# Optimization experiments

Measured on AMD Instinct MI355X. Metric: run time of the kernel, lower is better.

## Reference

```python
import jax, jax.numpy as jnp
import numpy as np

QLEN, KLEN, BSZ, NHEAD, DHEAD = 1024, 1024, 2, 16, 64
RLEN = QLEN + KLEN
SCALE = 1.0 / np.sqrt(DHEAD).astype(np.float32)  # 1/sqrt(d_head)


def setup_inputs() -> dict:
    key = jax.random.key(0)
    ks = jax.random.split(key, 10)
    return {
        "q_head": jax.random.normal(ks[0], (QLEN, BSZ, NHEAD, DHEAD), jnp.float32),
        "k_head_h": jax.random.normal(ks[1], (KLEN, BSZ, NHEAD, DHEAD), jnp.float32),
        "v_head_h": jax.random.normal(ks[2], (KLEN, BSZ, NHEAD, DHEAD), jnp.float32),
        "k_head_r": jax.random.normal(ks[3], (RLEN, BSZ, NHEAD, DHEAD), jnp.float32),
        "seg_embed": jax.random.normal(ks[4], (2, NHEAD, DHEAD), jnp.float32),
        "seg_mat": jax.random.uniform(ks[5], (QLEN, KLEN, BSZ, 2), jnp.float32),
        "r_w_bias": jax.random.normal(ks[6], (NHEAD, DHEAD), jnp.float32),
        "r_r_bias": jax.random.normal(ks[7], (NHEAD, DHEAD), jnp.float32),
        "r_s_bias": jax.random.normal(ks[8], (NHEAD, DHEAD), jnp.float32),
        "attn_mask": jnp.zeros((QLEN, KLEN, 1, 1), jnp.float32),
    }


def _rel_shift(x, klen):
    # x: [qlen, rlen, bsz, n_head] -> [qlen, klen, bsz, n_head]
    x = jnp.transpose(x, (1, 0, 2, 3))[1:]          # drop first position row
    x = jnp.transpose(x, (1, 0, 2, 3))[:, :klen]    # keep first klen columns
    return x


def reference(q_head, k_head_h, v_head_h, k_head_r, seg_embed, seg_mat,
              r_w_bias, r_r_bias, r_s_bias, attn_mask):
    # content-based score
    ac = jnp.einsum('ibnd,jbnd->ijbn', q_head + r_w_bias, k_head_h)
    # position-based score with relative shift
    bd = jnp.einsum('ibnd,jbnd->ijbn', q_head + r_r_bias, k_head_r)
    bd = _rel_shift(bd, klen=ac.shape[1])
    # segment-based score
    ef = jnp.einsum('ibnd,snd->ibns', q_head + r_s_bias, seg_embed)
    ef = jnp.einsum('ijbs,ibns->ijbn', seg_mat, ef)
    attn_score = (ac + bd + ef) * SCALE
    attn_score = attn_score - 1e30 * attn_mask
    attn_prob = jax.nn.softmax(attn_score, axis=1)  # over key dim j
    attn_vec = jnp.einsum('ijbn,jbnd->ibnd', attn_prob, v_head_h)
    return attn_vec
```

## Files before the change

kernel.cpp:

```cpp
#include <hip/hip_runtime.h>

#define QLEN 1024
#define KLEN 1024
#define BSZ 2
#define NHEAD 16
#define DHEAD 64
#define RS 2048
#define BLK_I 64
#define BLK_J 32
#define NT32 (KLEN / BLK_J)
#define NBN (BSZ * NHEAD)

#define SC2f  0.18033688011112440f
#define MBIGf 1.4426950408889634e30f

#define SEGP_BYTES  16777216u
#define KT_BYTES    ((size_t)NBN * NT32 * 4096)

typedef __attribute__((ext_vector_type(8))) short s16x8;
typedef __attribute__((ext_vector_type(8))) unsigned short u16x8;
typedef __attribute__((ext_vector_type(4))) unsigned short u16x4;
typedef __attribute__((ext_vector_type(4))) float f32x4;
typedef __attribute__((ext_vector_type(2))) float f32x2;

__device__ __forceinline__ unsigned short f2bf(float f) {
    union { float f; unsigned int u; } x; x.f = f;
    unsigned int r = x.u + 0x7fffu + ((x.u >> 16) & 1u);
    return (unsigned short)(r >> 16);
}
__device__ __forceinline__ float bf2f(unsigned short h) {
    union { unsigned int u; float f; } x; x.u = ((unsigned int)h) << 16;
    return x.f;
}

typedef const __attribute__((address_space(1))) unsigned int* gas_t;
typedef __attribute__((address_space(3))) unsigned int* las_t;
__device__ __forceinline__ void gl_lds16(const void* g, void* l) {
    __builtin_amdgcn_global_load_lds((gas_t)g, (las_t)l, 16, 0, 0);
}

__global__ __launch_bounds__(256)
void pack_all_kernel(const float* __restrict__ segmat,
                     const float* __restrict__ mask,
                     const float* __restrict__ kh,
                     const float* __restrict__ kr,
                     const float* __restrict__ v,
                     unsigned short* __restrict__ segT,
                     unsigned short* __restrict__ Kp,
                     unsigned short* __restrict__ Krp,
                     unsigned short* __restrict__ Vtp)
{
    __shared__ float smS[16][32][4];
    __shared__ float smM[16][33];
    __shared__ float VT[32][65];
    const int bid = blockIdx.x;
    const int tid = threadIdx.x;

    if (bid < 2048) {
        const int istrip = bid >> 5;
        const int jt     = bid & 31;
        const int ib     = istrip * 16;
        const int jb     = jt * 32;
        {
            const int il = tid >> 4;
            const int j2 = (tid & 15) * 2;
            const float* sp = segmat + ((size_t)(ib + il) * KLEN + jb + j2) * 4;
            *(f32x4*)&smS[il][j2][0]     = *(const f32x4*)sp;
            *(f32x4*)&smS[il][j2 + 1][0] = *(const f32x4*)(sp + 4);
            const float* mp = mask + (size_t)(ib + il) * KLEN + jb + j2;
            smM[il][j2]     = mp[0] * MBIGf;
            smM[il][j2 + 1] = mp[1] * MBIGf;
        }
        __syncthreads();
        const int k  = tid >> 6;
        const int l  = tid & 63;
        const int q4 = l >> 4;
        const int il = l & 15;
        const int jl = (k >> 1) * 16 + q4 * 4 + (k & 1) * 2;
#pragma unroll
        for (int b = 0; b < 2; ++b) {
            u16x8 o;
#pragma unroll
            for (int e = 0; e < 2; ++e) {
                o[e * 4 + 0] = f2bf(smS[il][jl + e][b * 2]);
                o[e * 4 + 1] = f2bf(smS[il][jl + e][b * 2 + 1]);
                o[e * 4 + 2] = f2bf(smM[il][jl + e]);
                o[e * 4 + 3] = 0;
            }
            unsigned short* op = segT + ((size_t)(b * 64 + istrip) << 16)
                                 + (jt << 11) + tid * 8;
            *(u16x8*)op = o;
        }
    } else {
        const int blk = bid - 2048;
        const int bn  = blk >> 5;
        const int jt  = blk & (NT32 - 1);
        const int b   = bn & 1;
        const int n   = bn >> 1;
        const int boff = b * NHEAD * DHEAD + n * DHEAD;
        const int j0  = jt * BLK_J;

        {
            const int j  = tid >> 3;
            const int dq = (tid & 7) * 8;
            const float* vp = v + (size_t)(j0 + j) * RS + boff + dq;
#pragma unroll
            for (int e = 0; e < 8; ++e) VT[j][dq + e] = vp[e];
        }
        __syncthreads();

        const size_t tb = (size_t)blk * 2048;
        {
            const int row = tid >> 3;
            const int ch  = (tid & 7) ^ (row & 7);
            u16x8 ok, orr;
            const float* hp = kh + (size_t)(j0 + row) * RS + boff + ch * 8;
            const float* rp = kr + (size_t)(j0 + row + 1) * RS + boff + ch * 8;
#pragma unroll
            for (int e = 0; e < 8; ++e) { ok[e] = f2bf(hp[e]); orr[e] = f2bf(rp[e]); }
            *(u16x8*)&Kp [tb + (size_t)tid * 8] = ok;
            *(u16x8*)&Krp[tb + (size_t)tid * 8] = orr;
        }
        {
            const int d  = tid >> 2;
            const int g  = tid & 3;
            const int ch = g ^ (d & 3);
            u16x8 ov;
#pragma unroll
            for (int e = 0; e < 8; ++e) ov[e] = f2bf(VT[ch * 8 + e][d]);
            *(u16x8*)&Vtp[tb + (size_t)tid * 8] = ov;
        }
    }
}

__global__ __launch_bounds__(256, 2)
void relattn_kernel(const float* __restrict__ q,
                    const float* __restrict__ segemb,
                    const float* __restrict__ rwb,
                    const float* __restrict__ rrb,
                    const float* __restrict__ rsb,
                    const unsigned short* __restrict__ segT,
                    const unsigned short* __restrict__ Kp,
                    const unsigned short* __restrict__ Krp,
                    const unsigned short* __restrict__ Vtp,
                    float* __restrict__ out)
{
    __shared__ unsigned short KhL[2][32][64];
    __shared__ unsigned short KrL[2][32][64];
    __shared__ unsigned short VtL[2][64][32];
    __shared__ unsigned short PlP[4][16][40];

    const int F = blockIdx.x;
    const int x = F & 7;
    const int k = F >> 3;
    const int g = (k >> 4) * 8 + x;
    const int i0 = (g >> 1) * BLK_I;
    const int b  = g & 1;
    const int n  = k & 15;
    const int bn = n * 2 + b;
    const int boff = b * NHEAD * DHEAD + n * DHEAD;

    const int tid  = threadIdx.x;
    const int wave = tid >> 6;
    const int lane = tid & 63;
    const int q4   = lane >> 4;
    const int c    = lane & 15;
    const int iRow = i0 + wave * 16 + c;

    s16x8 qwf[2], qrf[2];
    float e0, e1;
    {
        const float* qp = q + (size_t)iRow * RS + boff;
        float es0 = 0.f, es1 = 0.f;
#pragma unroll
        for (int kk = 0; kk < 2; ++kk) {
            const int off = kk * 32 + q4 * 8;
            const f32x4 q0 = *(const f32x4*)(qp + off);
            const f32x4 q1 = *(const f32x4*)(qp + off + 4);
            const f32x4 w0 = *(const f32x4*)(rwb + n * DHEAD + off);
            const f32x4 w1 = *(const f32x4*)(rwb + n * DHEAD + off + 4);
            const f32x4 r0 = *(const f32x4*)(rrb + n * DHEAD + off);
            const f32x4 r1 = *(const f32x4*)(rrb + n * DHEAD + off + 4);
            const f32x4 sa = *(const f32x4*)(segemb + n * DHEAD + off);
            const f32x4 sb = *(const f32x4*)(segemb + n * DHEAD + off + 4);
            const f32x4 ta = *(const f32x4*)(segemb + (NHEAD + n) * DHEAD + off);
            const f32x4 tb = *(const f32x4*)(segemb + (NHEAD + n) * DHEAD + off + 4);
            const f32x4 ra = *(const f32x4*)(rsb + n * DHEAD + off);
            const f32x4 rb = *(const f32x4*)(rsb + n * DHEAD + off + 4);
            s16x8 tw, tr;
#pragma unroll
            for (int e = 0; e < 4; ++e) {
                tw[e]     = (short)f2bf(q0[e] + w0[e]);
                tw[4 + e] = (short)f2bf(q1[e] + w1[e]);
                tr[e]     = (short)f2bf(q0[e] + r0[e]);
                tr[4 + e] = (short)f2bf(q1[e] + r1[e]);
                es0 += (q0[e] + ra[e]) * sa[e] + (q1[e] + rb[e]) * sb[e];
                es1 += (q0[e] + ra[e]) * ta[e] + (q1[e] + rb[e]) * tb[e];
            }
            qwf[kk] = tw; qrf[kk] = tr;
        }
        es0 += __shfl_xor(es0, 16, 64); es0 += __shfl_xor(es0, 32, 64);
        es1 += __shfl_xor(es1, 16, 64); es1 += __shfl_xor(es1, 32, 64);
        e0 = es0 * SC2f; e1 = es1 * SC2f;
    }

    const int tbase = bn * NT32;
    auto stage = [&](int jt, int buf) {
        const size_t toff = ((size_t)(tbase + jt)) << 12;
        const int go = tid * 16;
        const int lo = wave * 1024;
        gl_lds16((const char*)Kp  + toff + go, (char*)&KhL[buf][0][0] + lo);
        gl_lds16((const char*)Krp + toff + go, (char*)&KrL[buf][0][0] + lo);
        gl_lds16((const char*)Vtp + toff + go, (char*)&VtL[buf][0][0] + lo);
    };

    stage(0, 0);
    __syncthreads();

    float m = -INFINITY, lsum = 0.f;
    f32x4 acc[4];
#pragma unroll
    for (int dt = 0; dt < 4; ++dt) acc[dt] = (f32x4)0.f;

    const unsigned short* segW = segT + ((size_t)(b * 64 + (i0 >> 4) + wave) << 16);

    int cur = 0;
    for (int jt = 0; jt < NT32; ++jt) {
        if (jt + 1 < NT32) stage(jt + 1, cur ^ 1);

        const unsigned short* st = segW + (jt << 11);
        u16x8 pg[2][2];
        pg[0][0] = *(const u16x8*)(st + lane * 8);
        pg[0][1] = *(const u16x8*)(st + 512 + lane * 8);
        pg[1][0] = *(const u16x8*)(st + 1024 + lane * 8);
        pg[1][1] = *(const u16x8*)(st + 1536 + lane * 8);

        f32x4 sjT[2];
        sjT[0] = (f32x4)0.f; sjT[1] = (f32x4)0.f;
        __builtin_amdgcn_s_setprio(1);
#pragma unroll
        for (int kk = 0; kk < 2; ++kk)
#pragma unroll
            for (int js = 0; js < 2; ++js) {
                const int row = js * 16 + c;
                const int pcK = ((kk * 4 + q4) ^ (c & 7)) * 8;
                const s16x8 khf = *(const s16x8*)&KhL[cur][row][pcK];
                const s16x8 krf = *(const s16x8*)&KrL[cur][row][pcK];
                sjT[js] = __builtin_amdgcn_mfma_f32_16x16x32_bf16(khf, qwf[kk], sjT[js], 0, 0, 0);
                sjT[js] = __builtin_amdgcn_mfma_f32_16x16x32_bf16(krf, qrf[kk], sjT[js], 0, 0, 0);
            }
        __builtin_amdgcn_s_setprio(0);

        float sc8[8];
#pragma unroll
        for (int js = 0; js < 2; ++js)
#pragma unroll
            for (int r = 0; r < 4; ++r) {
                const u16x8 g2 = pg[js][r >> 1];
                const int bb = (r & 1) * 4;
                sc8[js * 4 + r] = sjT[js][r] * SC2f
                                  + bf2f(g2[bb]) * e0 + bf2f(g2[bb + 1]) * e1
                                  - bf2f(g2[bb + 2]);
            }
        float mt = fmaxf(
            fmaxf(fmaxf(sc8[0], sc8[1]), fmaxf(sc8[2], sc8[3])),
            fmaxf(fmaxf(sc8[4], sc8[5]), fmaxf(sc8[6], sc8[7])));
        mt = fmaxf(mt, __shfl_xor(mt, 16, 64));
        mt = fmaxf(mt, __shfl_xor(mt, 32, 64));
        const float mn  = fmaxf(m, mt);
        const float scl = __builtin_amdgcn_exp2f(m - mn);
        m = mn;
#pragma unroll
        for (int dt = 0; dt < 4; ++dt) acc[dt] *= scl;
        float p[8], ps = 0.f;
#pragma unroll
        for (int e = 0; e < 8; ++e) {
            p[e] = __builtin_amdgcn_exp2f(sc8[e] - m);
            ps += p[e];
        }
        lsum = lsum * scl + ps;

#pragma unroll
        for (int js = 0; js < 2; ++js) {
            unsigned int wlo, whi;
            asm("v_cvt_pk_bf16_f32 %0, %1, %2" : "=v"(wlo) : "v"(p[js * 4 + 0]), "v"(p[js * 4 + 1]));
            asm("v_cvt_pk_bf16_f32 %0, %1, %2" : "=v"(whi) : "v"(p[js * 4 + 2]), "v"(p[js * 4 + 3]));
            uint2 wv; wv.x = wlo; wv.y = whi;
            *(uint2*)((char*)&PlP[wave][c][0] + js * 32 + q4 * 8) = wv;
        }
        const s16x8 pf = *(const s16x8*)&PlP[wave][c][q4 * 8];

        __builtin_amdgcn_s_setprio(1);
#pragma unroll
        for (int dt = 0; dt < 4; ++dt) {
            const s16x8 vf = *(const s16x8*)&VtL[cur][dt * 16 + c][(q4 ^ (c & 3)) * 8];
            acc[dt] = __builtin_amdgcn_mfma_f32_16x16x32_bf16(vf, pf, acc[dt], 0, 0, 0);
        }
        __builtin_amdgcn_s_setprio(0);

        __syncthreads();
        cur ^= 1;
    }

    lsum += __shfl_xor(lsum, 16, 64);
    lsum += __shfl_xor(lsum, 32, 64);

    {
        const float inv = 1.f / lsum;
        float* op = out + (size_t)iRow * RS + boff;
#pragma unroll
        for (int dt = 0; dt < 4; ++dt) {
            const f32x4 o = acc[dt] * inv;
            *(f32x4*)&op[dt * 16 + q4 * 4] = o;
        }
    }
}

extern "C" void kernel_launch(void* const* d_in, const int* in_sizes, int n_in,
                              void* d_out, int out_size, void* d_ws, size_t ws_size,
                              hipStream_t stream) {
    const float* q   = (const float*)d_in[0];
    const float* kh  = (const float*)d_in[1];
    const float* v   = (const float*)d_in[2];
    const float* kr  = (const float*)d_in[3];
    const float* se  = (const float*)d_in[4];
    const float* sm  = (const float*)d_in[5];
    const float* rwb = (const float*)d_in[6];
    const float* rrb = (const float*)d_in[7];
    const float* rsb = (const float*)d_in[8];
    const float* msk = (const float*)d_in[9];
    float* out = (float*)d_out;

    char* wsb = (char*)d_ws;
    unsigned short* segT = (unsigned short*)wsb;
    unsigned short* Kp   = (unsigned short*)(wsb + SEGP_BYTES);
    unsigned short* Krp  = (unsigned short*)(wsb + SEGP_BYTES + KT_BYTES);
    unsigned short* Vtp  = (unsigned short*)(wsb + SEGP_BYTES + 2 * KT_BYTES);

    pack_all_kernel<<<2048 + NBN * NT32, 256, 0, stream>>>(sm, msk, kh, kr, v,
                                                           segT, Kp, Krp, Vtp);
    relattn_kernel<<<512, 256, 0, stream>>>(q, se, rwb, rrb, rsb, segT, Kp, Krp, Vtp, out);
}
```

Before: 56.10 us.

## Split key range across two blocks with merge kernel and lazy softmax rescale

Adds a split-K (flash-decoding style) path. Each query tile's key range is divided between two blocks, which write partial outputs plus max/sum values to workspace, and a new merge kernel combines them. The grid doubles to 1024 blocks and occupancy is raised to 4 blocks per CU, to fill the GPU better with the original 512 blocks. The online softmax now skips the rescale unless the running max grows by more than a threshold. The costs are an extra kernel launch and a partial-result round-trip through global memory.

```diff
diff --git a/kernel.cpp b/kernel.cpp
--- a/kernel.cpp
+++ b/kernel.cpp
@@ -13,9 +13,12 @@
 
 #define SC2f  0.18033688011112440f
 #define MBIGf 1.4426950408889634e30f
+#define THRf  8.0f
 
 #define SEGP_BYTES  16777216u
 #define KT_BYTES    ((size_t)NBN * NT32 * 4096)
+#define OPART_BYTES 16777216u
+#define ML_BYTES    524288u
 
 typedef __attribute__((ext_vector_type(8))) short s16x8;
 typedef __attribute__((ext_vector_type(8))) unsigned short u16x8;
@@ -133,7 +136,30 @@
     }
 }
 
-__global__ __launch_bounds__(256, 2)
+__global__ __launch_bounds__(256)
+void merge_kernel(const float* __restrict__ opart,
+                  const float* __restrict__ ml,
+                  float* __restrict__ out)
+{
+    const int gid = blockIdx.x * 256 + threadIdx.x;
+    const int d   = gid & 63;
+    const int rr  = gid >> 6;
+    const int i   = rr & (QLEN - 1);
+    const int n   = (rr >> 10) & (NHEAD - 1);
+    const int b   = rr >> 14;
+    const int r0  = rr;
+    const int r1  = (NBN * QLEN) + rr;
+    const float m0 = ml[r0 * 2], l0 = ml[r0 * 2 + 1];
+    const float m1 = ml[r1 * 2], l1 = ml[r1 * 2 + 1];
+    const float M  = fmaxf(m0, m1);
+    const float w0 = __builtin_amdgcn_exp2f(m0 - M);
+    const float w1 = __builtin_amdgcn_exp2f(m1 - M);
+    const float inv = 1.f / (l0 * w0 + l1 * w1);
+    const float o = (opart[(size_t)r0 * 64 + d] * w0 + opart[(size_t)r1 * 64 + d] * w1) * inv;
+    out[(size_t)i * RS + b * NHEAD * DHEAD + n * DHEAD + d] = o;
+}
+
+__global__ __launch_bounds__(256, 4)
 void relattn_kernel(const float* __restrict__ q,
                     const float* __restrict__ segemb,
                     const float* __restrict__ rwb,
@@ -143,7 +169,10 @@
                     const unsigned short* __restrict__ Kp,
                     const unsigned short* __restrict__ Krp,
                     const unsigned short* __restrict__ Vtp,
-                    float* __restrict__ out)
+                    float* __restrict__ opart,
+                    float* __restrict__ mlpart,
+                    float* __restrict__ out,
+                    int jsplit, int njt)
 {
     __shared__ unsigned short KhL[2][32][64];
     __shared__ unsigned short KrL[2][32][64];
@@ -154,9 +183,10 @@
     const int x = F & 7;
     const int k = F >> 3;
     const int g = (k >> 4) * 8 + x;
-    const int i0 = (g >> 1) * BLK_I;
-    const int b  = g & 1;
-    const int n  = k & 15;
+    const int n = k & 15;
+    int i0, b, jsp;
+    if (jsplit) { i0 = (g >> 2) * BLK_I; b = (g >> 1) & 1; jsp = g & 1; }
+    else        { i0 = (g >> 1) * BLK_I; b = g & 1;        jsp = 0;    }
     const int bn = n * 2 + b;
     const int boff = b * NHEAD * DHEAD + n * DHEAD;
 
@@ -204,7 +234,7 @@
         e0 = es0 * SC2f; e1 = es1 * SC2f;
     }
 
-    const int tbase = bn * NT32;
+    const int tbase = bn * NT32 + jsp * njt;
     auto stage = [&](int jt, int buf) {
         const size_t toff = ((size_t)(tbase + jt)) << 12;
         const int go = tid * 16;
@@ -225,10 +255,10 @@
     const unsigned short* segW = segT + ((size_t)(b * 64 + (i0 >> 4) + wave) << 16);
 
     int cur = 0;
-    for (int jt = 0; jt < NT32; ++jt) {
-        if (jt + 1 < NT32) stage(jt + 1, cur ^ 1);
-
-        const unsigned short* st = segW + (jt << 11);
+    for (int jt = 0; jt < njt; ++jt) {
+        if (jt + 1 < njt) stage(jt + 1, cur ^ 1);
+
+        const unsigned short* st = segW + ((jsp * njt + jt) << 11);
         u16x8 pg[2][2];
         pg[0][0] = *(const u16x8*)(st + lane * 8);
         pg[0][1] = *(const u16x8*)(st + 512 + lane * 8);
@@ -262,23 +292,29 @@
                                   + bf2f(g2[bb]) * e0 + bf2f(g2[bb + 1]) * e1
                                   - bf2f(g2[bb + 2]);
             }
-        float mt = fmaxf(
+        float pmax = fmaxf(
             fmaxf(fmaxf(sc8[0], sc8[1]), fmaxf(sc8[2], sc8[3])),
             fmaxf(fmaxf(sc8[4], sc8[5]), fmaxf(sc8[6], sc8[7])));
-        mt = fmaxf(mt, __shfl_xor(mt, 16, 64));
-        mt = fmaxf(mt, __shfl_xor(mt, 32, 64));
-        const float mn  = fmaxf(m, mt);
-        const float scl = __builtin_amdgcn_exp2f(m - mn);
-        m = mn;
-#pragma unroll
-        for (int dt = 0; dt < 4; ++dt) acc[dt] *= scl;
+
+        if (!__all(pmax <= m + THRf)) {
+            float mt = pmax;
+            mt = fmaxf(mt, __shfl_xor(mt, 16, 64));
+            mt = fmaxf(mt, __shfl_xor(mt, 32, 64));
+            const float mn  = fmaxf(m, mt);
+            const float scl = __builtin_amdgcn_exp2f(m - mn);
+            m = mn;
+            lsum *= scl;
+#pragma unroll
+            for (int dt = 0; dt < 4; ++dt) acc[dt] *= scl;
+        }
+
         float p[8], ps = 0.f;
 #pragma unroll
         for (int e = 0; e < 8; ++e) {
             p[e] = __builtin_amdgcn_exp2f(sc8[e] - m);
             ps += p[e];
         }
-        lsum = lsum * scl + ps;
+        lsum += ps;
 
 #pragma unroll
         for (int js = 0; js < 2; ++js) {
@@ -305,7 +341,16 @@
     lsum += __shfl_xor(lsum, 16, 64);
     lsum += __shfl_xor(lsum, 32, 64);
 
-    {
+    if (jsplit) {
+        const int rowG = ((jsp * BSZ + b) * NHEAD + n) * QLEN + iRow;
+#pragma unroll
+        for (int dt = 0; dt < 4; ++dt)
+            *(f32x4*)&opart[(size_t)rowG * 64 + dt * 16 + q4 * 4] = acc[dt];
+        if (q4 == 0) {
+            mlpart[(size_t)rowG * 2]     = m;
+            mlpart[(size_t)rowG * 2 + 1] = lsum;
+        }
+    } else {
         const float inv = 1.f / lsum;
         float* op = out + (size_t)iRow * RS + boff;
 #pragma unroll
@@ -336,8 +381,18 @@
     unsigned short* Kp   = (unsigned short*)(wsb + SEGP_BYTES);
     unsigned short* Krp  = (unsigned short*)(wsb + SEGP_BYTES + KT_BYTES);
     unsigned short* Vtp  = (unsigned short*)(wsb + SEGP_BYTES + 2 * KT_BYTES);
+    float* opart  = (float*)(wsb + SEGP_BYTES + 3 * KT_BYTES);
+    float* mlpart = (float*)(wsb + SEGP_BYTES + 3 * KT_BYTES + OPART_BYTES);
+
+    const int jsplit = (ws_size >= (size_t)SEGP_BYTES + 3 * KT_BYTES + OPART_BYTES + ML_BYTES) ? 1 : 0;
+    const int njt    = jsplit ? NT32 / 2 : NT32;
 
     pack_all_kernel<<<2048 + NBN * NT32, 256, 0, stream>>>(sm, msk, kh, kr, v,
                                                            segT, Kp, Krp, Vtp);
-    relattn_kernel<<<512, 256, 0, stream>>>(q, se, rwb, rrb, rsb, segT, Kp, Krp, Vtp, out);
-}
+    relattn_kernel<<<jsplit ? 1024 : 512, 256, 0, stream>>>(q, se, rwb, rrb, rsb,
+                                                            segT, Kp, Krp, Vtp,
+                                                            opart, mlpart, out,
+                                                            jsplit, njt);
+    if (jsplit)
+        merge_kernel<<<NBN * QLEN * DHEAD / 256, 256, 0, stream>>>(opart, mlpart, out);
+}
```

Measured after the change: 57.76 us. 3.0% more time.

## Split key tiles across wave pairs with lazy rescale and 16x16x16 PV MFMA

Applied to the files above, without the earlier changes.

Halves the query block to 32 rows and assigns each pair of waves to split the 32-key tile, so each wave computes one 16x16 score block. Partial softmax states are merged through LDS at the end. This doubles the grid to 1024 blocks and raises the occupancy target to 4. It also skips the running-max rescale unless the new max exceeds the old one by a threshold. P is fed straight from registers into a 16x16x16 bf16 MFMA, which removes the LDS round-trip for P, and the V pack layout changes to match. The cost is more blocks each reloading K/V tiles, extra merge work, and more exp range headroom.

```diff
diff --git a/kernel.cpp b/kernel.cpp
--- a/kernel.cpp
+++ b/kernel.cpp
@@ -6,18 +6,20 @@
 #define NHEAD 16
 #define DHEAD 64
 #define RS 2048
-#define BLK_I 64
+#define BLK_I 32
 #define BLK_J 32
 #define NT32 (KLEN / BLK_J)
 #define NBN (BSZ * NHEAD)
 
 #define SC2f  0.18033688011112440f
 #define MBIGf 1.4426950408889634e30f
+#define THRf  8.0f
 
 #define SEGP_BYTES  16777216u
 #define KT_BYTES    ((size_t)NBN * NT32 * 4096)
 
 typedef __attribute__((ext_vector_type(8))) short s16x8;
+typedef __attribute__((ext_vector_type(4))) short s16x4;
 typedef __attribute__((ext_vector_type(8))) unsigned short u16x8;
 typedef __attribute__((ext_vector_type(4))) unsigned short u16x4;
 typedef __attribute__((ext_vector_type(4))) float f32x4;
@@ -31,6 +33,17 @@
 __device__ __forceinline__ float bf2f(unsigned short h) {
     union { unsigned int u; float f; } x; x.u = ((unsigned int)h) << 16;
     return x.f;
+}
+
+__device__ __forceinline__ f32x4 mfma16x16x16(s16x4 a, s16x4 b, f32x4 c) {
+#if __has_builtin(__builtin_amdgcn_mfma_f32_16x16x16bf16_1k)
+    return __builtin_amdgcn_mfma_f32_16x16x16bf16_1k(a, b, c, 0, 0, 0);
+#else
+    f32x4 d;
+    asm("v_mfma_f32_16x16x16_bf16 %0, %1, %2, %3"
+        : "=v"(d) : "v"(a), "v"(b), "0"(c));
+    return d;
+#endif
 }
 
 typedef const __attribute__((address_space(1))) unsigned int* gas_t;
@@ -123,17 +136,21 @@
         }
         {
             const int d  = tid >> 2;
-            const int g  = tid & 3;
-            const int ch = g ^ (d & 3);
-            u16x8 ov;
-#pragma unroll
-            for (int e = 0; e < 8; ++e) ov[e] = f2bf(VT[ch * 8 + e][d]);
-            *(u16x8*)&Vtp[tb + (size_t)tid * 8] = ov;
-        }
-    }
-}
-
-__global__ __launch_bounds__(256, 2)
+            const int gl = tid & 3;
+#pragma unroll
+            for (int s = 0; s < 2; ++s) {
+                const int gj8 = gl * 2 + s;
+                const int ph  = gj8 ^ (d & 7);
+                u16x4 ov;
+#pragma unroll
+                for (int e = 0; e < 4; ++e) ov[e] = f2bf(VT[gj8 * 4 + e][d]);
+                *(u16x4*)&Vtp[tb + (size_t)d * 32 + ph * 4] = ov;
+            }
+        }
+    }
+}
+
+__global__ __launch_bounds__(256, 4)
 void relattn_kernel(const float* __restrict__ q,
                     const float* __restrict__ segemb,
                     const float* __restrict__ rwb,
@@ -148,16 +165,16 @@
     __shared__ unsigned short KhL[2][32][64];
     __shared__ unsigned short KrL[2][32][64];
     __shared__ unsigned short VtL[2][64][32];
-    __shared__ unsigned short PlP[4][16][40];
-
-    const int F = blockIdx.x;
-    const int x = F & 7;
-    const int k = F >> 3;
-    const int g = (k >> 4) * 8 + x;
-    const int i0 = (g >> 1) * BLK_I;
-    const int b  = g & 1;
-    const int n  = k & 15;
-    const int bn = n * 2 + b;
+
+    const int F  = blockIdx.x;
+    const int x  = F & 7;
+    const int k2 = F >> 3;
+    const int g  = (k2 >> 4) * 8 + x;
+    const int n  = k2 & 15;
+    const int it32 = g >> 1;
+    const int b    = g & 1;
+    const int i0   = it32 * BLK_I;
+    const int bn   = n * 2 + b;
     const int boff = b * NHEAD * DHEAD + n * DHEAD;
 
     const int tid  = threadIdx.x;
@@ -165,7 +182,9 @@
     const int lane = tid & 63;
     const int q4   = lane >> 4;
     const int c    = lane & 15;
-    const int iRow = i0 + wave * 16 + c;
+    const int ih   = wave >> 1;
+    const int jh   = wave & 1;
+    const int iRow = i0 + ih * 16 + c;
 
     s16x8 qwf[2], qrf[2];
     float e0, e1;
@@ -222,79 +241,74 @@
 #pragma unroll
     for (int dt = 0; dt < 4; ++dt) acc[dt] = (f32x4)0.f;
 
-    const unsigned short* segW = segT + ((size_t)(b * 64 + (i0 >> 4) + wave) << 16);
+    const unsigned short* segW = segT + ((size_t)(b * 64 + it32 * 2 + ih) << 16);
 
     int cur = 0;
     for (int jt = 0; jt < NT32; ++jt) {
         if (jt + 1 < NT32) stage(jt + 1, cur ^ 1);
 
         const unsigned short* st = segW + (jt << 11);
-        u16x8 pg[2][2];
-        pg[0][0] = *(const u16x8*)(st + lane * 8);
-        pg[0][1] = *(const u16x8*)(st + 512 + lane * 8);
-        pg[1][0] = *(const u16x8*)(st + 1024 + lane * 8);
-        pg[1][1] = *(const u16x8*)(st + 1536 + lane * 8);
-
-        f32x4 sjT[2];
-        sjT[0] = (f32x4)0.f; sjT[1] = (f32x4)0.f;
+        u16x8 pg2[2];
+        pg2[0] = *(const u16x8*)(st + (jh * 2 + 0) * 512 + lane * 8);
+        pg2[1] = *(const u16x8*)(st + (jh * 2 + 1) * 512 + lane * 8);
+
+        f32x4 sjT = (f32x4)0.f;
         __builtin_amdgcn_s_setprio(1);
 #pragma unroll
-        for (int kk = 0; kk < 2; ++kk)
-#pragma unroll
-            for (int js = 0; js < 2; ++js) {
-                const int row = js * 16 + c;
-                const int pcK = ((kk * 4 + q4) ^ (c & 7)) * 8;
-                const s16x8 khf = *(const s16x8*)&KhL[cur][row][pcK];
-                const s16x8 krf = *(const s16x8*)&KrL[cur][row][pcK];
-                sjT[js] = __builtin_amdgcn_mfma_f32_16x16x32_bf16(khf, qwf[kk], sjT[js], 0, 0, 0);
-                sjT[js] = __builtin_amdgcn_mfma_f32_16x16x32_bf16(krf, qrf[kk], sjT[js], 0, 0, 0);
-            }
+        for (int kk = 0; kk < 2; ++kk) {
+            const int row = jh * 16 + c;
+            const int pcK = ((kk * 4 + q4) ^ (c & 7)) * 8;
+            const s16x8 khf = *(const s16x8*)&KhL[cur][row][pcK];
+            const s16x8 krf = *(const s16x8*)&KrL[cur][row][pcK];
+            sjT = __builtin_amdgcn_mfma_f32_16x16x32_bf16(khf, qwf[kk], sjT, 0, 0, 0);
+            sjT = __builtin_amdgcn_mfma_f32_16x16x32_bf16(krf, qrf[kk], sjT, 0, 0, 0);
+        }
         __builtin_amdgcn_s_setprio(0);
 
-        float sc8[8];
-#pragma unroll
-        for (int js = 0; js < 2; ++js)
-#pragma unroll
-            for (int r = 0; r < 4; ++r) {
-                const u16x8 g2 = pg[js][r >> 1];
-                const int bb = (r & 1) * 4;
-                sc8[js * 4 + r] = sjT[js][r] * SC2f
-                                  + bf2f(g2[bb]) * e0 + bf2f(g2[bb + 1]) * e1
-                                  - bf2f(g2[bb + 2]);
-            }
-        float mt = fmaxf(
-            fmaxf(fmaxf(sc8[0], sc8[1]), fmaxf(sc8[2], sc8[3])),
-            fmaxf(fmaxf(sc8[4], sc8[5]), fmaxf(sc8[6], sc8[7])));
-        mt = fmaxf(mt, __shfl_xor(mt, 16, 64));
-        mt = fmaxf(mt, __shfl_xor(mt, 32, 64));
-        const float mn  = fmaxf(m, mt);
-        const float scl = __builtin_amdgcn_exp2f(m - mn);
-        m = mn;
-#pragma unroll
-        for (int dt = 0; dt < 4; ++dt) acc[dt] *= scl;
-        float p[8], ps = 0.f;
-#pragma unroll
-        for (int e = 0; e < 8; ++e) {
-            p[e] = __builtin_amdgcn_exp2f(sc8[e] - m);
+        float sc4[4];
+#pragma unroll
+        for (int r = 0; r < 4; ++r) {
+            const u16x8 g2 = pg2[r >> 1];
+            const int bb = (r & 1) * 4;
+            sc4[r] = sjT[r] * SC2f
+                     + bf2f(g2[bb]) * e0 + bf2f(g2[bb + 1]) * e1
+                     - bf2f(g2[bb + 2]);
+        }
+        float pmax = fmaxf(fmaxf(sc4[0], sc4[1]), fmaxf(sc4[2], sc4[3]));
+
+        if (!__all(pmax <= m + THRf)) {
+            float mt = pmax;
+            mt = fmaxf(mt, __shfl_xor(mt, 16, 64));
+            mt = fmaxf(mt, __shfl_xor(mt, 32, 64));
+            const float mn  = fmaxf(m, mt);
+            const float scl = __builtin_amdgcn_exp2f(m - mn);
+            m = mn;
+            lsum *= scl;
+#pragma unroll
+            for (int dt = 0; dt < 4; ++dt) acc[dt] *= scl;
+        }
+
+        float p[4], ps = 0.f;
+#pragma unroll
+        for (int e = 0; e < 4; ++e) {
+            p[e] = __builtin_amdgcn_exp2f(sc4[e] - m);
             ps += p[e];
         }
-        lsum = lsum * scl + ps;
-
-#pragma unroll
-        for (int js = 0; js < 2; ++js) {
-            unsigned int wlo, whi;
-            asm("v_cvt_pk_bf16_f32 %0, %1, %2" : "=v"(wlo) : "v"(p[js * 4 + 0]), "v"(p[js * 4 + 1]));
-            asm("v_cvt_pk_bf16_f32 %0, %1, %2" : "=v"(whi) : "v"(p[js * 4 + 2]), "v"(p[js * 4 + 3]));
-            uint2 wv; wv.x = wlo; wv.y = whi;
-            *(uint2*)((char*)&PlP[wave][c][0] + js * 32 + q4 * 8) = wv;
-        }
-        const s16x8 pf = *(const s16x8*)&PlP[wave][c][q4 * 8];
-
+        lsum += ps;
+
+        s16x4 pf4;
+        {
+            union { unsigned int w[2]; s16x4 v; } pk2;
+            asm("v_cvt_pk_bf16_f32 %0, %1, %2" : "=v"(pk2.w[0]) : "v"(p[0]), "v"(p[1]));
+            asm("v_cvt_pk_bf16_f32 %0, %1, %2" : "=v"(pk2.w[1]) : "v"(p[2]), "v"(p[3]));
+            pf4 = pk2.v;
+        }
         __builtin_amdgcn_s_setprio(1);
 #pragma unroll
         for (int dt = 0; dt < 4; ++dt) {
-            const s16x8 vf = *(const s16x8*)&VtL[cur][dt * 16 + c][(q4 ^ (c & 3)) * 8];
-            acc[dt] = __builtin_amdgcn_mfma_f32_16x16x32_bf16(vf, pf, acc[dt], 0, 0, 0);
+            const int ph = (jh * 4 + q4) ^ (c & 7);
+            const s16x4 vf = *(const s16x4*)&VtL[cur][dt * 16 + c][ph * 4];
+            acc[dt] = mfma16x16x16(vf, pf4, acc[dt]);
         }
         __builtin_amdgcn_s_setprio(0);
 
@@ -305,12 +319,33 @@
     lsum += __shfl_xor(lsum, 16, 64);
     lsum += __shfl_xor(lsum, 32, 64);
 
-    {
-        const float inv = 1.f / lsum;
+    __syncthreads();
+    float* scrO  = (float*)&KhL[0][0][0];
+    float* scrML = (float*)&VtL[0][0][0];
+    if (jh == 1) {
+        const int rowL = ih * 16 + c;
+#pragma unroll
+        for (int dt = 0; dt < 4; ++dt)
+            *(f32x4*)&scrO[rowL * 68 + dt * 16 + q4 * 4] = acc[dt];
+        if (q4 == 0) {
+            scrML[rowL * 2]     = m;
+            scrML[rowL * 2 + 1] = lsum;
+        }
+    }
+    __syncthreads();
+    if (jh == 0) {
+        const int rowL = ih * 16 + c;
+        const float m1 = scrML[rowL * 2];
+        const float l1 = scrML[rowL * 2 + 1];
+        const float M  = fmaxf(m, m1);
+        const float w0 = __builtin_amdgcn_exp2f(m - M);
+        const float w1 = __builtin_amdgcn_exp2f(m1 - M);
+        const float inv = 1.f / (lsum * w0 + l1 * w1);
         float* op = out + (size_t)iRow * RS + boff;
 #pragma unroll
         for (int dt = 0; dt < 4; ++dt) {
-            const f32x4 o = acc[dt] * inv;
+            const f32x4 o = (acc[dt] * w0
+                          + (*(const f32x4*)&scrO[rowL * 68 + dt * 16 + q4 * 4]) * w1) * inv;
             *(f32x4*)&op[dt * 16 + q4 * 4] = o;
         }
     }
@@ -339,5 +374,6 @@
 
     pack_all_kernel<<<2048 + NBN * NT32, 256, 0, stream>>>(sm, msk, kh, kr, v,
                                                            segT, Kp, Krp, Vtp);
-    relattn_kernel<<<512, 256, 0, stream>>>(q, se, rwb, rrb, rsb, segT, Kp, Krp, Vtp, out);
-}
+    relattn_kernel<<<1024, 256, 0, stream>>>(q, se, rwb, rrb, rsb,
+                                             segT, Kp, Krp, Vtp, out);
+}
```

Measured after the change: 56.43 us. No clear change (+0.6%).
